# Performance work log

Measured on AMD Instinct MI355X. Metric: run time of the kernel, lower is better.

## Reference

```python
import jax, jax.numpy as jnp
import numpy as np

PATCH, STRIDE, TOPK, EPS = 16, 8, 8, 1e-8

def _leaky(x):
    return jax.nn.leaky_relu(x, 0.01)

def setup_inputs() -> dict:
    key = jax.random.key(0)
    ks = jax.random.split(key, 12)
    s = 0.05  # small weight scale to avoid tanh saturation
    return {
        "X":      jax.random.normal(ks[0], (16, 4096, 512), jnp.float32),
        "W_enc1": jax.random.normal(ks[1], (512, 256), jnp.float32) * s,
        "b_enc1": jax.random.normal(ks[2], (256,), jnp.float32) * s,
        "W_enc2": jax.random.normal(ks[3], (256, 64), jnp.float32) * s,
        "b_enc2": jax.random.normal(ks[4], (64,), jnp.float32) * s,
        "Wq":     jax.random.normal(ks[5], (64, 64), jnp.float32) * s,
        "Wk":     jax.random.normal(ks[6], (64, 64), jnp.float32) * s,
        "Wv":     jax.random.normal(ks[7], (64, 64), jnp.float32) * s,
        "W_agg":  jax.random.normal(ks[8], (64, 64), jnp.float32) * s,
        "b_agg":  jax.random.normal(ks[9], (64,), jnp.float32) * s,
        "W_dec":  jax.random.normal(ks[10], (64, 512), jnp.float32) * s,
        "b_dec":  jax.random.normal(ks[11], (512,), jnp.float32) * s,
    }

def reference(X, W_enc1, b_enc1, W_enc2, b_enc2, Wq, Wk, Wv, W_agg, b_agg, W_dec, b_dec):
    B, L, D = X.shape
    # var_encoder (dropout-free MLP)
    Xe = _leaky(X @ W_enc1 + b_enc1) @ W_enc2 + b_enc2          # (B, L, d)
    d = Xe.shape[-1]
    # unfold into overlapping patches
    h = (L - PATCH) // STRIDE + 1
    pos = jnp.arange(h)[:, None] * STRIDE + jnp.arange(PATCH)[None, :]  # (h, PATCH)
    patches = Xe[:, pos, :]                                      # (B, h, PATCH, d)
    per_patch = patches.mean(axis=2).reshape(B * h, d)           # (N, d)
    q = per_patch @ Wq
    k = per_patch @ Wk
    v = per_patch @ Wv                                           # (N, hqk)
    qn = q / (jnp.linalg.norm(q, axis=-1, keepdims=True) + EPS)
    kn = k / (jnp.linalg.norm(k, axis=-1, keepdims=True) + EPS)
    # antisymmetric outer product, (N, hqk, hqk)
    M = qn[:, :, None] * kn[:, None, :] - kn[:, :, None] * qn[:, None, :]
    A = jax.nn.relu(jnp.tanh(M))
    n = A.shape[-1]
    # topk pruning along last dim via scatter-style mask
    _, idx = jax.lax.top_k(A, TOPK)                              # (N, n, TOPK)
    mask = jnp.any(idx[..., None] == jnp.arange(n), axis=-2)     # (N, n, n) bool
    A = A * mask.astype(A.dtype)
    A = A / jnp.maximum(A.sum(axis=-1, keepdims=True), EPS)
    Av = jnp.einsum('nij,nj->ni', A, v)                          # (N, hqk)
    # after_agg (dropout = identity in eval)
    z = _leaky(Av @ W_agg + b_agg)                               # (N, d)
    zB = z.reshape(B, h, d)
    # overlap-add fold: each patch writes its (constant-over-time) z to its window
    seg = jnp.broadcast_to(zB[:, :, None, :], (B, h, PATCH, d)).reshape(B, h * PATCH, d)
    flat_pos = pos.reshape(-1)                                   # (h*PATCH,)
    out = jnp.zeros((B, L, d), X.dtype).at[:, flat_pos, :].add(seg)
    counts = jnp.zeros((L,), X.dtype).at[flat_pos].add(1.0)
    out = out / jnp.maximum(counts, 1.0)[None, :, None]
    return out @ W_dec + b_dec                                   # (B, L, D)
```

## Files before the change

kernel.cpp:

```cpp
#include <hip/hip_runtime.h>


typedef __attribute__((ext_vector_type(8))) _Float16 half8;
typedef __attribute__((ext_vector_type(4))) _Float16 half4;
typedef __attribute__((ext_vector_type(4))) float floatx4;

__device__ __forceinline__ _Float16 f2h(float f) { return (_Float16)f; }

__global__ __launch_bounds__(256) void prep_weights(
    const float* __restrict__ W1, const float* __restrict__ W2,
    const float* __restrict__ Wd,
    _Float16* __restrict__ W1t, _Float16* __restrict__ W2t,
    _Float16* __restrict__ Wdt)
{
    int idx = blockIdx.x * 256 + threadIdx.x;
    { int n = idx >> 9, k = idx & 511;  W1t[idx] = f2h(W1[k * 256 + n]); }
    if (idx < 16384) { int n = idx >> 8, k = idx & 255; W2t[idx] = f2h(W2[k * 64 + n]); }
    if (idx < 32768) { int n = idx >> 6, k = idx & 63;  Wdt[idx] = f2h(Wd[k * 512 + n]); }
}

template<int BM, int BN, int WM, int WN, bool AF32, int EPI>
__global__ __launch_bounds__(256) void gemm_kernel(
    const void* __restrict__ Aq, const _Float16* __restrict__ Bt,
    const float* __restrict__ bias, void* __restrict__ Cq,
    int M, int N, int K, int lda)
{
    constexpr int LDK = 72;
    __shared__ _Float16 As[BM * LDK];
    __shared__ _Float16 Bs[BN * LDK];
    static_assert(32 * BN * 4 <= BM * LDK * 2, "epilogue chunk must fit in As");

    const int tid  = threadIdx.x;
    const int lane = tid & 63;
    const int w    = tid >> 6;
    constexpr int MWAVES = BM / WM;
    const int wrow = (w % MWAVES) * WM;
    const int wcol = (w / MWAVES) * WN;
    constexpr int MI = WM / 16, NI = WN / 16;
    const int m0 = blockIdx.y * BM;
    const int n0 = blockIdx.x * BN;

    floatx4 acc[MI][NI];
#pragma unroll
    for (int a = 0; a < MI; a++)
#pragma unroll
        for (int bq = 0; bq < NI; bq++) acc[a][bq] = (floatx4){0.f, 0.f, 0.f, 0.f};

    constexpr int EPTA = BM * 64 / 256;
    constexpr int TPRA = 64 / EPTA;
    const int arow  = tid / TPRA;
    const int akseg = (tid % TPRA) * EPTA;
    constexpr int EPTB = BN * 64 / 256;
    constexpr int TPRB = 64 / EPTB;
    const int brow  = tid / TPRB;
    const int bkseg = (tid % TPRB) * EPTB;

    const float*    Af = (const float*)Aq;
    const _Float16* Ah = (const _Float16*)Aq;

    float4 pa[AF32 ? EPTA / 4 : 1];
    half8  paq[AF32 ? 1 : EPTA / 8];
    half8  pb[EPTB / 8];

    auto loadA = [&](int kt) {
        if constexpr (AF32) {
            const float* s = Af + (size_t)(m0 + arow) * lda + kt + akseg;
#pragma unroll
            for (int u = 0; u < EPTA / 4; u++) pa[u] = *(const float4*)(s + 4 * u);
        } else {
            const _Float16* s = Ah + (size_t)(m0 + arow) * lda + kt + akseg;
#pragma unroll
            for (int u = 0; u < EPTA / 8; u++) paq[u] = *(const half8*)(s + 8 * u);
        }
    };
    auto loadB = [&](int kt) {
        const _Float16* s = Bt + (size_t)(n0 + brow) * K + kt + bkseg;
#pragma unroll
        for (int u = 0; u < EPTB / 8; u++) pb[u] = *(const half8*)(s + 8 * u);
    };
    auto stage = [&]() {
        _Float16* d = &As[arow * LDK + akseg];
        if constexpr (AF32) {
#pragma unroll
            for (int u = 0; u < EPTA / 8; u++) {
                float4 f0 = pa[2 * u], f1 = pa[2 * u + 1];
                half8 o;
                o[0] = f2h(f0.x); o[1] = f2h(f0.y); o[2] = f2h(f0.z); o[3] = f2h(f0.w);
                o[4] = f2h(f1.x); o[5] = f2h(f1.y); o[6] = f2h(f1.z); o[7] = f2h(f1.w);
                *(half8*)(d + 8 * u) = o;
            }
        } else {
#pragma unroll
            for (int u = 0; u < EPTA / 8; u++) *(half8*)(d + 8 * u) = paq[u];
        }
        _Float16* db = &Bs[brow * LDK + bkseg];
#pragma unroll
        for (int u = 0; u < EPTB / 8; u++) *(half8*)(db + 8 * u) = pb[u];
    };

    loadA(0); loadB(0);
    for (int kt = 0; kt < K; kt += 64) {
        stage();
        __syncthreads();
        if (kt + 64 < K) { loadA(kt + 64); loadB(kt + 64); }
#pragma unroll
        for (int ks = 0; ks < 2; ks++) {
            const int koff = ks * 32 + (lane >> 4) * 8;
            half8 af[MI], bf[NI];
#pragma unroll
            for (int mi = 0; mi < MI; mi++)
                af[mi] = *(const half8*)&As[(wrow + mi * 16 + (lane & 15)) * LDK + koff];
#pragma unroll
            for (int ni = 0; ni < NI; ni++)
                bf[ni] = *(const half8*)&Bs[(wcol + ni * 16 + (lane & 15)) * LDK + koff];
#pragma unroll
            for (int mi = 0; mi < MI; mi++)
#pragma unroll
                for (int ni = 0; ni < NI; ni++)
                    acc[mi][ni] = __builtin_amdgcn_mfma_f32_16x16x32_f16(
                        af[mi], bf[ni], acc[mi][ni], 0, 0, 0);
        }
        __syncthreads();
    }

    float bvv[NI];
#pragma unroll
    for (int ni = 0; ni < NI; ni++) bvv[ni] = bias[n0 + wcol + ni * 16 + (lane & 15)];

    float* Cs = (float*)As;
#pragma unroll
    for (int c = 0; c < BM / 32; c++) {
        __syncthreads();
        constexpr int DUMMY = 0; (void)DUMMY;
        {
            const int own_wrow = ((c * 32) / WM) * WM;
            if (wrow == own_wrow) {
                constexpr int CPW = 32 < WM ? 32 : WM;
#pragma unroll
                for (int mm = 0; mm < CPW / 16; mm++) {
                    const int mi = ((c * 32) % WM) / 16 + mm;
#pragma unroll
                    for (int ni = 0; ni < NI; ni++) {
#pragma unroll
                        for (int r = 0; r < 4; r++) {
                            const int lr  = mm * 16 + (lane >> 4) * 4 + r;
                            const int col = wcol + ni * 16 + (lane & 15);
                            Cs[lr * BN + col] = acc[mi][ni][r] + bvv[ni];
                        }
                    }
                }
            }
        }
        __syncthreads();
#pragma unroll
        for (int u = 0; u < (32 * BN) / 1024; u++) {
            const int idx = (u * 256 + tid) * 4;
            const int lr = idx / BN, col = idx - lr * BN;
            float4 vv = *(const float4*)&Cs[idx];
            const size_t go = (size_t)(m0 + c * 32 + lr) * N + n0 + col;
            if constexpr (EPI == 0) {
                half4 hv;
                hv[0] = f2h(vv.x > 0.f ? vv.x : 0.01f * vv.x);
                hv[1] = f2h(vv.y > 0.f ? vv.y : 0.01f * vv.y);
                hv[2] = f2h(vv.z > 0.f ? vv.z : 0.01f * vv.z);
                hv[3] = f2h(vv.w > 0.f ? vv.w : 0.01f * vv.w);
                *(half4*)((_Float16*)Cq + go) = hv;
            } else {
                *(float4*)((float*)Cq + go) = vv;
            }
        }
    }
}

#define TOP8_INS(mv) do { float _x = (mv); float _t;            \
    _t = fmaxf(s0,_x); _x = fminf(s0,_x); s0 = _t;              \
    _t = fmaxf(s1,_x); _x = fminf(s1,_x); s1 = _t;              \
    _t = fmaxf(s2,_x); _x = fminf(s2,_x); s2 = _t;              \
    _t = fmaxf(s3,_x); _x = fminf(s3,_x); s3 = _t;              \
    _t = fmaxf(s4,_x); _x = fminf(s4,_x); s4 = _t;              \
    _t = fmaxf(s5,_x); _x = fminf(s5,_x); s5 = _t;              \
    _t = fmaxf(s6,_x); _x = fminf(s6,_x); s6 = _t;              \
    s7 = fmaxf(s7,_x); } while (0)

__global__ __launch_bounds__(256) void patch_attn(
    const float* __restrict__ Xe,  const float* __restrict__ Wq,
    const float* __restrict__ Wk,  const float* __restrict__ Wv,
    const float* __restrict__ Wagg, const float* __restrict__ bagg,
    float* __restrict__ zout)
{
    __shared__ float sh[4][336];
    const int w    = threadIdx.x >> 6;
    const int lane = threadIdx.x & 63;
    const int n = blockIdx.x * 4 + w;
    const int b = n / 511;
    const int i = n - b * 511;
    float* pp  = &sh[w][0];
    float* qs  = pp + 64;
    float* ksm = pp + 128;
    float* vsm = pp + 192;
    float* avs = pp + 256;

    const float* xb = Xe + ((size_t)(b * 4096 + i * 8)) * 64 + lane;
    float s = 0.f;
#pragma unroll
    for (int p = 0; p < 16; p++) s += xb[(size_t)p * 64];
    pp[lane] = s * 0.0625f;
    __syncthreads();

    float q = 0.f, k = 0.f, v = 0.f;
#pragma unroll 4
    for (int e = 0; e < 64; e += 4) {
        float4 p4 = *(const float4*)&pp[e];
        q = fmaf(p4.x, Wq[(e+0)*64+lane], q); q = fmaf(p4.y, Wq[(e+1)*64+lane], q);
        q = fmaf(p4.z, Wq[(e+2)*64+lane], q); q = fmaf(p4.w, Wq[(e+3)*64+lane], q);
        k = fmaf(p4.x, Wk[(e+0)*64+lane], k); k = fmaf(p4.y, Wk[(e+1)*64+lane], k);
        k = fmaf(p4.z, Wk[(e+2)*64+lane], k); k = fmaf(p4.w, Wk[(e+3)*64+lane], k);
        v = fmaf(p4.x, Wv[(e+0)*64+lane], v); v = fmaf(p4.y, Wv[(e+1)*64+lane], v);
        v = fmaf(p4.z, Wv[(e+2)*64+lane], v); v = fmaf(p4.w, Wv[(e+3)*64+lane], v);
    }
    float sq = q * q, sk = k * k;
#pragma unroll
    for (int o = 1; o < 64; o <<= 1) { sq += __shfl_xor(sq, o); sk += __shfl_xor(sk, o); }
    const float qni = q / (sqrtf(sq) + 1e-8f);
    const float kni = k / (sqrtf(sk) + 1e-8f);
    qs[lane] = qni; ksm[lane] = kni; vsm[lane] = v;
    __syncthreads();

    auto MV = [&](float kj, float qj) { return fmaf(qni, kj, -(kni * qj)); };

    float s0=-1e30f,s1=-1e30f,s2=-1e30f,s3=-1e30f,s4=-1e30f,s5=-1e30f,s6=-1e30f,s7=-1e30f;
#pragma unroll
    for (int j = 0; j < 64; j += 4) {
        float4 k4 = *(const float4*)&ksm[j];
        float4 q4 = *(const float4*)&qs[j];
        TOP8_INS(MV(k4.x, q4.x)); TOP8_INS(MV(k4.y, q4.y));
        TOP8_INS(MV(k4.z, q4.z)); TOP8_INS(MV(k4.w, q4.w));
    }
    const float teff = fmaxf(s7, 1e-37f) * (1.f - 1.2e-7f);

    float ssum = 0.f, av = 0.f;
#pragma unroll
    for (int j = 0; j < 64; j += 4) {
        float4 k4 = *(const float4*)&ksm[j];
        float4 q4 = *(const float4*)&qs[j];
        float4 v4 = *(const float4*)&vsm[j];
#define P2(KJ, QJ, VJ) do { float _m = MV(KJ, QJ); float _x2 = _m * _m;           \
        float _a = _m * (15.f + _x2) * __builtin_amdgcn_rcpf(fmaf(6.f, _x2, 15.f)); \
        float _am = (_m >= teff) ? _a : 0.f;                                       \
        ssum += _am; av = fmaf(_am, (VJ), av); } while (0)
        P2(k4.x, q4.x, v4.x); P2(k4.y, q4.y, v4.y);
        P2(k4.z, q4.z, v4.z); P2(k4.w, q4.w, v4.w);
#undef P2
    }
    avs[lane] = av / fmaxf(ssum, 1e-8f);
    __syncthreads();

    float zc = bagg[lane];
#pragma unroll 4
    for (int e = 0; e < 64; e += 4) {
        float4 a4 = *(const float4*)&avs[e];
        zc = fmaf(a4.x, Wagg[(e+0)*64+lane], zc); zc = fmaf(a4.y, Wagg[(e+1)*64+lane], zc);
        zc = fmaf(a4.z, Wagg[(e+2)*64+lane], zc); zc = fmaf(a4.w, Wagg[(e+3)*64+lane], zc);
    }
    zc = zc > 0.f ? zc : 0.01f * zc;
    zout[(size_t)n * 64 + lane] = zc;
}

__global__ __launch_bounds__(256) void scatter_avg(
    const float* __restrict__ z, _Float16* __restrict__ zavg)
{
    const int idx = blockIdx.x * 256 + threadIdx.x;
    const int c = idx & 63;
    const int l = (idx >> 6) & 4095;
    const int b = idx >> 18;
    const int g = l >> 3;
    float s = 0.f, cnt = 0.f;
    if (g >= 1)   { s += z[((size_t)(b * 511 + g - 1)) * 64 + c]; cnt += 1.f; }
    if (g <= 510) { s += z[((size_t)(b * 511 + g)) * 64 + c];     cnt += 1.f; }
    zavg[idx] = f2h(s / cnt);
}

extern "C" void kernel_launch(void* const* d_in, const int* in_sizes, int n_in,
                              void* d_out, int out_size, void* d_ws, size_t ws_size,
                              hipStream_t stream)
{
    const float* X    = (const float*)d_in[0];
    const float* W1   = (const float*)d_in[1];
    const float* b1   = (const float*)d_in[2];
    const float* W2   = (const float*)d_in[3];
    const float* b2   = (const float*)d_in[4];
    const float* Wq   = (const float*)d_in[5];
    const float* Wk   = (const float*)d_in[6];
    const float* Wv   = (const float*)d_in[7];
    const float* Wagg = (const float*)d_in[8];
    const float* bagg = (const float*)d_in[9];
    const float* Wd   = (const float*)d_in[10];
    const float* bd   = (const float*)d_in[11];

    char* ws = (char*)d_ws;
    _Float16* hidden = (_Float16*)(ws);
    float*    Xe     = (float*)(ws + 33554432);
    float*    z      = (float*)(ws + 50331648);
    _Float16* zavg   = (_Float16*)(ws + 52424704);
    _Float16* W1t    = (_Float16*)(ws + 60813312);
    _Float16* W2t    = (_Float16*)(ws + 61075456);
    _Float16* Wdt    = (_Float16*)(ws + 61108224);
    float* out = (float*)d_out;

    prep_weights<<<512, 256, 0, stream>>>(W1, W2, Wd, W1t, W2t, Wdt);

    gemm_kernel<128,128,64,64,true,0><<<dim3(2,512), 256, 0, stream>>>(
        X, W1t, b1, hidden, 65536, 256, 512, 512);
    gemm_kernel<128,64,32,64,false,1><<<dim3(1,512), 256, 0, stream>>>(
        hidden, W2t, b2, Xe, 65536, 64, 256, 256);
    patch_attn<<<2044, 256, 0, stream>>>(Xe, Wq, Wk, Wv, Wagg, bagg, z);
    scatter_avg<<<16384, 256, 0, stream>>>(z, zavg);
    gemm_kernel<128,128,64,64,false,1><<<dim3(4,512), 256, 0, stream>>>(
        zavg, Wdt, bd, out, 65536, 512, 64, 64);
}
```

Baseline: 341.2 us.

## Fuse encoder GEMMs in one kernel and fold scatter-average into decoder

Merges the two encoder GEMMs into one kernel. Each block computes a 64-row hidden tile (all 256 columns) and keeps it in shared memory for the second GEMM, so the fp16 hidden tensor never goes through global memory. W1 tiles are loaded straight into LDS with global_load_lds using an XOR swizzle. The overlap-add averaging is computed inside the decoder's A-tile load, which removes the scatter_avg kernel and the zavg buffer. The costs are higher shared-memory use per block and a less parallel grid for the first GEMM, since each block now covers all 256 columns.

```diff
diff --git a/kernel.cpp b/kernel.cpp
--- a/kernel.cpp
+++ b/kernel.cpp
@@ -6,6 +6,8 @@
 typedef __attribute__((ext_vector_type(4))) float floatx4;
 
 __device__ __forceinline__ _Float16 f2h(float f) { return (_Float16)f; }
+
+#define MFMA16(A, B, C) __builtin_amdgcn_mfma_f32_16x16x32_f16((A), (B), (C), 0, 0, 0)
 
 __global__ __launch_bounds__(256) void prep_weights(
     const float* __restrict__ W1, const float* __restrict__ W2,
@@ -19,155 +21,136 @@
     if (idx < 32768) { int n = idx >> 6, k = idx & 63;  Wdt[idx] = f2h(Wd[k * 512 + n]); }
 }
 
-template<int BM, int BN, int WM, int WN, bool AF32, int EPI>
-__global__ __launch_bounds__(256) void gemm_kernel(
-    const void* __restrict__ Aq, const _Float16* __restrict__ Bt,
-    const float* __restrict__ bias, void* __restrict__ Cq,
-    int M, int N, int K, int lda)
-{
-    constexpr int LDK = 72;
-    __shared__ _Float16 As[BM * LDK];
-    __shared__ _Float16 Bs[BN * LDK];
-    static_assert(32 * BN * 4 <= BM * LDK * 2, "epilogue chunk must fit in As");
+__global__ __launch_bounds__(256) void enc_fused(
+    const float* __restrict__ X, const _Float16* __restrict__ W1t,
+    const float* __restrict__ b1, const _Float16* __restrict__ W2t,
+    const float* __restrict__ b2, float* __restrict__ Xe)
+{
+    __shared__ _Float16 smem[21504];
+    _Float16* As  = smem;
+    _Float16* Bs  = smem + 4608;
+    _Float16* Hs  = smem;
+    _Float16* W2s = smem + 16896;
 
     const int tid  = threadIdx.x;
     const int lane = tid & 63;
     const int w    = tid >> 6;
-    constexpr int MWAVES = BM / WM;
-    const int wrow = (w % MWAVES) * WM;
-    const int wcol = (w / MWAVES) * WN;
-    constexpr int MI = WM / 16, NI = WN / 16;
-    const int m0 = blockIdx.y * BM;
-    const int n0 = blockIdx.x * BN;
-
-    floatx4 acc[MI][NI];
-#pragma unroll
-    for (int a = 0; a < MI; a++)
-#pragma unroll
-        for (int bq = 0; bq < NI; bq++) acc[a][bq] = (floatx4){0.f, 0.f, 0.f, 0.f};
-
-    constexpr int EPTA = BM * 64 / 256;
-    constexpr int TPRA = 64 / EPTA;
-    const int arow  = tid / TPRA;
-    const int akseg = (tid % TPRA) * EPTA;
-    constexpr int EPTB = BN * 64 / 256;
-    constexpr int TPRB = 64 / EPTB;
-    const int brow  = tid / TPRB;
-    const int bkseg = (tid % TPRB) * EPTB;
-
-    const float*    Af = (const float*)Aq;
-    const _Float16* Ah = (const _Float16*)Aq;
-
-    float4 pa[AF32 ? EPTA / 4 : 1];
-    half8  paq[AF32 ? 1 : EPTA / 8];
-    half8  pb[EPTB / 8];
-
+    const int m0   = blockIdx.x * 64;
+
+    const int arow  = tid >> 2;
+    const int akseg = (tid & 3) << 4;
+    const float* Abase = X + (size_t)(m0 + arow) * 512 + akseg;
+
+    const int brow0  = (w << 6) + (lane >> 3);
+    const int bchunk = (((lane & 7) ^ ((lane >> 3) & 7)) << 3);
+
+    floatx4 acc1[4][4];
+#pragma unroll
+    for (int ci = 0; ci < 4; ci++)
+#pragma unroll
+        for (int mi = 0; mi < 4; mi++) acc1[ci][mi] = (floatx4){0.f, 0.f, 0.f, 0.f};
+
+    float4 pa[4];
     auto loadA = [&](int kt) {
-        if constexpr (AF32) {
-            const float* s = Af + (size_t)(m0 + arow) * lda + kt + akseg;
-#pragma unroll
-            for (int u = 0; u < EPTA / 4; u++) pa[u] = *(const float4*)(s + 4 * u);
-        } else {
-            const _Float16* s = Ah + (size_t)(m0 + arow) * lda + kt + akseg;
-#pragma unroll
-            for (int u = 0; u < EPTA / 8; u++) paq[u] = *(const half8*)(s + 8 * u);
-        }
+#pragma unroll
+        for (int u = 0; u < 4; u++) pa[u] = *(const float4*)(Abase + kt + 4 * u);
     };
-    auto loadB = [&](int kt) {
-        const _Float16* s = Bt + (size_t)(n0 + brow) * K + kt + bkseg;
-#pragma unroll
-        for (int u = 0; u < EPTB / 8; u++) pb[u] = *(const half8*)(s + 8 * u);
-    };
-    auto stage = [&]() {
-        _Float16* d = &As[arow * LDK + akseg];
-        if constexpr (AF32) {
-#pragma unroll
-            for (int u = 0; u < EPTA / 8; u++) {
-                float4 f0 = pa[2 * u], f1 = pa[2 * u + 1];
+
+    loadA(0);
+    for (int kt = 0; kt < 512; kt += 64) {
+#pragma unroll
+        for (int inst = 0; inst < 8; inst++) {
+            const _Float16* src = W1t + (size_t)(brow0 + inst * 8) * 512 + kt + bchunk;
+            __builtin_amdgcn_global_load_lds(
+                (const __attribute__((address_space(1))) unsigned int*)src,
+                (__attribute__((address_space(3))) unsigned int*)(Bs + ((w << 6) + inst * 8) * 64),
+                16, 0, 0);
+        }
+        {
+            _Float16* d = &As[arow * 72 + akseg];
+#pragma unroll
+            for (int h = 0; h < 2; h++) {
+                float4 f0 = pa[2 * h], f1 = pa[2 * h + 1];
                 half8 o;
                 o[0] = f2h(f0.x); o[1] = f2h(f0.y); o[2] = f2h(f0.z); o[3] = f2h(f0.w);
                 o[4] = f2h(f1.x); o[5] = f2h(f1.y); o[6] = f2h(f1.z); o[7] = f2h(f1.w);
-                *(half8*)(d + 8 * u) = o;
+                *(half8*)(d + 8 * h) = o;
             }
-        } else {
-#pragma unroll
-            for (int u = 0; u < EPTA / 8; u++) *(half8*)(d + 8 * u) = paq[u];
-        }
-        _Float16* db = &Bs[brow * LDK + bkseg];
-#pragma unroll
-        for (int u = 0; u < EPTB / 8; u++) *(half8*)(db + 8 * u) = pb[u];
-    };
-
-    loadA(0); loadB(0);
-    for (int kt = 0; kt < K; kt += 64) {
-        stage();
-        __syncthreads();
-        if (kt + 64 < K) { loadA(kt + 64); loadB(kt + 64); }
+        }
+        __syncthreads();
+        if (kt + 64 < 512) loadA(kt + 64);
 #pragma unroll
         for (int ks = 0; ks < 2; ks++) {
-            const int koff = ks * 32 + (lane >> 4) * 8;
-            half8 af[MI], bf[NI];
-#pragma unroll
-            for (int mi = 0; mi < MI; mi++)
-                af[mi] = *(const half8*)&As[(wrow + mi * 16 + (lane & 15)) * LDK + koff];
-#pragma unroll
-            for (int ni = 0; ni < NI; ni++)
-                bf[ni] = *(const half8*)&Bs[(wcol + ni * 16 + (lane & 15)) * LDK + koff];
-#pragma unroll
-            for (int mi = 0; mi < MI; mi++)
-#pragma unroll
-                for (int ni = 0; ni < NI; ni++)
-                    acc[mi][ni] = __builtin_amdgcn_mfma_f32_16x16x32_f16(
-                        af[mi], bf[ni], acc[mi][ni], 0, 0, 0);
-        }
-        __syncthreads();
-    }
-
-    float bvv[NI];
-#pragma unroll
-    for (int ni = 0; ni < NI; ni++) bvv[ni] = bias[n0 + wcol + ni * 16 + (lane & 15)];
-
-    float* Cs = (float*)As;
-#pragma unroll
-    for (int c = 0; c < BM / 32; c++) {
-        __syncthreads();
-        constexpr int DUMMY = 0; (void)DUMMY;
-        {
-            const int own_wrow = ((c * 32) / WM) * WM;
-            if (wrow == own_wrow) {
-                constexpr int CPW = 32 < WM ? 32 : WM;
-#pragma unroll
-                for (int mm = 0; mm < CPW / 16; mm++) {
-                    const int mi = ((c * 32) % WM) / 16 + mm;
-#pragma unroll
-                    for (int ni = 0; ni < NI; ni++) {
-#pragma unroll
-                        for (int r = 0; r < 4; r++) {
-                            const int lr  = mm * 16 + (lane >> 4) * 4 + r;
-                            const int col = wcol + ni * 16 + (lane & 15);
-                            Cs[lr * BN + col] = acc[mi][ni][r] + bvv[ni];
-                        }
-                    }
-                }
+            const int lchunk = ks * 4 + (lane >> 4);
+            half8 af[4], bf[4];
+#pragma unroll
+            for (int ci = 0; ci < 4; ci++) {
+                const int c = (w << 6) + ci * 16 + (lane & 15);
+                af[ci] = *(const half8*)&Bs[c * 64 + ((lchunk ^ (lane & 7)) << 3)];
             }
-        }
-        __syncthreads();
-#pragma unroll
-        for (int u = 0; u < (32 * BN) / 1024; u++) {
-            const int idx = (u * 256 + tid) * 4;
-            const int lr = idx / BN, col = idx - lr * BN;
-            float4 vv = *(const float4*)&Cs[idx];
-            const size_t go = (size_t)(m0 + c * 32 + lr) * N + n0 + col;
-            if constexpr (EPI == 0) {
-                half4 hv;
-                hv[0] = f2h(vv.x > 0.f ? vv.x : 0.01f * vv.x);
-                hv[1] = f2h(vv.y > 0.f ? vv.y : 0.01f * vv.y);
-                hv[2] = f2h(vv.z > 0.f ? vv.z : 0.01f * vv.z);
-                hv[3] = f2h(vv.w > 0.f ? vv.w : 0.01f * vv.w);
-                *(half4*)((_Float16*)Cq + go) = hv;
-            } else {
-                *(float4*)((float*)Cq + go) = vv;
+#pragma unroll
+            for (int mi = 0; mi < 4; mi++)
+                bf[mi] = *(const half8*)&As[(mi * 16 + (lane & 15)) * 72 + ks * 32 + ((lane >> 4) << 3)];
+#pragma unroll
+            for (int ci = 0; ci < 4; ci++)
+#pragma unroll
+                for (int mi = 0; mi < 4; mi++)
+                    acc1[ci][mi] = MFMA16(af[ci], bf[mi], acc1[ci][mi]);
+        }
+        __syncthreads();
+    }
+
+    float4 b1v[4];
+#pragma unroll
+    for (int ci = 0; ci < 4; ci++)
+        b1v[ci] = *(const float4*)&b1[(w << 6) + ci * 16 + ((lane >> 4) << 2)];
+#pragma unroll
+    for (int ci = 0; ci < 4; ci++) {
+        const int cb = (w << 6) + ci * 16 + ((lane >> 4) << 2);
+#pragma unroll
+        for (int mi = 0; mi < 4; mi++) {
+            const int m = mi * 16 + (lane & 15);
+            half4 hv;
+#pragma unroll
+            for (int r = 0; r < 4; r++) {
+                float v = acc1[ci][mi][r] + ((const float*)&b1v[ci])[r];
+                v = v > 0.f ? v : 0.01f * v;
+                hv[r] = f2h(v);
             }
+            *(half4*)&Hs[m * 264 + cb] = hv;
+        }
+    }
+
+    floatx4 acc2[4];
+#pragma unroll
+    for (int ni = 0; ni < 4; ni++) acc2[ni] = (floatx4){0.f, 0.f, 0.f, 0.f};
+    const int w2n   = tid >> 2;
+    const int w2seg = (tid & 3) << 4;
+#pragma unroll
+    for (int p = 0; p < 4; p++) {
+        *(half8*)&W2s[w2n * 72 + w2seg]     = *(const half8*)&W2t[w2n * 256 + p * 64 + w2seg];
+        *(half8*)&W2s[w2n * 72 + w2seg + 8] = *(const half8*)&W2t[w2n * 256 + p * 64 + w2seg + 8];
+        __syncthreads();
+#pragma unroll
+        for (int ks = 0; ks < 2; ks++) {
+            half8 a2 = *(const half8*)&Hs[((w << 4) + (lane & 15)) * 264 + p * 64 + ks * 32 + ((lane >> 4) << 3)];
+            half8 b2f[4];
+#pragma unroll
+            for (int ni = 0; ni < 4; ni++)
+                b2f[ni] = *(const half8*)&W2s[(ni * 16 + (lane & 15)) * 72 + ks * 32 + ((lane >> 4) << 3)];
+#pragma unroll
+            for (int ni = 0; ni < 4; ni++)
+                acc2[ni] = MFMA16(a2, b2f[ni], acc2[ni]);
+        }
+        __syncthreads();
+    }
+#pragma unroll
+    for (int ni = 0; ni < 4; ni++) {
+        const float bb = b2[ni * 16 + (lane & 15)];
+#pragma unroll
+        for (int r = 0; r < 4; r++) {
+            const int row = m0 + (w << 4) + ((lane >> 4) << 2) + r;
+            Xe[(size_t)row * 64 + ni * 16 + (lane & 15)] = acc2[ni][r] + bb;
         }
     }
 }
@@ -266,18 +249,116 @@
     zout[(size_t)n * 64 + lane] = zc;
 }
 
-__global__ __launch_bounds__(256) void scatter_avg(
-    const float* __restrict__ z, _Float16* __restrict__ zavg)
-{
-    const int idx = blockIdx.x * 256 + threadIdx.x;
-    const int c = idx & 63;
-    const int l = (idx >> 6) & 4095;
-    const int b = idx >> 18;
-    const int g = l >> 3;
-    float s = 0.f, cnt = 0.f;
-    if (g >= 1)   { s += z[((size_t)(b * 511 + g - 1)) * 64 + c]; cnt += 1.f; }
-    if (g <= 510) { s += z[((size_t)(b * 511 + g)) * 64 + c];     cnt += 1.f; }
-    zavg[idx] = f2h(s / cnt);
+__global__ __launch_bounds__(256) void dec_fused(
+    const float* __restrict__ z, const _Float16* __restrict__ Wdt,
+    const float* __restrict__ bd, float* __restrict__ out)
+{
+    __shared__ _Float16 As[128 * 72];
+    __shared__ _Float16 Bs[128 * 72];
+    const int tid  = threadIdx.x;
+    const int lane = tid & 63;
+    const int w    = tid >> 6;
+    const int m0 = blockIdx.y * 128, n0 = blockIdx.x * 128;
+    const int wrow = (w & 1) << 6, wcol = (w >> 1) << 6;
+
+    {
+        const int arow  = tid >> 1;
+        const int akseg = (tid & 1) << 5;
+        const int row = m0 + arow;
+        const int b = row >> 12, l = row & 4095, g = l >> 3;
+        const int g0 = g - 1 >= 0 ? g - 1 : 0;
+        const int g1 = g <= 510 ? g : 510;
+        const float w0 = (g >= 1) ? 1.f : 0.f;
+        const float w1 = (g <= 510) ? 1.f : 0.f;
+        const float sc = (w0 + w1) > 1.5f ? 0.5f : 1.f;
+        const float* z0 = z + ((size_t)(b * 511 + g0)) * 64 + akseg;
+        const float* z1 = z + ((size_t)(b * 511 + g1)) * 64 + akseg;
+        _Float16* d = &As[arow * 72 + akseg];
+#pragma unroll
+        for (int u = 0; u < 4; u++) {
+            float4 f0a = *(const float4*)(z0 + 8 * u);
+            float4 f0b = *(const float4*)(z0 + 8 * u + 4);
+            float4 f1a = *(const float4*)(z1 + 8 * u);
+            float4 f1b = *(const float4*)(z1 + 8 * u + 4);
+            half8 o;
+            o[0] = f2h((f0a.x * w0 + f1a.x * w1) * sc);
+            o[1] = f2h((f0a.y * w0 + f1a.y * w1) * sc);
+            o[2] = f2h((f0a.z * w0 + f1a.z * w1) * sc);
+            o[3] = f2h((f0a.w * w0 + f1a.w * w1) * sc);
+            o[4] = f2h((f0b.x * w0 + f1b.x * w1) * sc);
+            o[5] = f2h((f0b.y * w0 + f1b.y * w1) * sc);
+            o[6] = f2h((f0b.z * w0 + f1b.z * w1) * sc);
+            o[7] = f2h((f0b.w * w0 + f1b.w * w1) * sc);
+            *(half8*)(d + 8 * u) = o;
+        }
+    }
+    {
+        const int brow  = tid >> 1;
+        const int bkseg = (tid & 1) << 5;
+        const _Float16* s = Wdt + (size_t)(n0 + brow) * 64 + bkseg;
+        _Float16* d = &Bs[brow * 72 + bkseg];
+#pragma unroll
+        for (int u = 0; u < 4; u++) *(half8*)(d + 8 * u) = *(const half8*)(s + 8 * u);
+    }
+    __syncthreads();
+
+    floatx4 acc[2][4];
+    floatx4 accf[4][4];
+#pragma unroll
+    for (int mi = 0; mi < 4; mi++)
+#pragma unroll
+        for (int ni = 0; ni < 4; ni++) accf[mi][ni] = (floatx4){0.f, 0.f, 0.f, 0.f};
+    (void)acc;
+#pragma unroll
+    for (int ks = 0; ks < 2; ks++) {
+        const int koff = ks * 32 + ((lane >> 4) << 3);
+        half8 af[4], bf[4];
+#pragma unroll
+        for (int mi = 0; mi < 4; mi++)
+            af[mi] = *(const half8*)&As[(wrow + mi * 16 + (lane & 15)) * 72 + koff];
+#pragma unroll
+        for (int ni = 0; ni < 4; ni++)
+            bf[ni] = *(const half8*)&Bs[(wcol + ni * 16 + (lane & 15)) * 72 + koff];
+#pragma unroll
+        for (int mi = 0; mi < 4; mi++)
+#pragma unroll
+            for (int ni = 0; ni < 4; ni++)
+                accf[mi][ni] = MFMA16(af[mi], bf[ni], accf[mi][ni]);
+    }
+
+    float bvv[4];
+#pragma unroll
+    for (int ni = 0; ni < 4; ni++) bvv[ni] = bd[n0 + wcol + ni * 16 + (lane & 15)];
+
+    float* Cs = (float*)As;
+#pragma unroll
+    for (int c = 0; c < 4; c++) {
+        __syncthreads();
+        const int own_wrow = ((c * 32) / 64) * 64;
+        if (wrow == own_wrow) {
+#pragma unroll
+            for (int mm = 0; mm < 2; mm++) {
+                const int mi = ((c * 32) % 64) / 16 + mm;
+#pragma unroll
+                for (int ni = 0; ni < 4; ni++) {
+#pragma unroll
+                    for (int r = 0; r < 4; r++) {
+                        const int lr  = mm * 16 + ((lane >> 4) << 2) + r;
+                        const int col = wcol + ni * 16 + (lane & 15);
+                        Cs[lr * 128 + col] = accf[mi][ni][r] + bvv[ni];
+                    }
+                }
+            }
+        }
+        __syncthreads();
+#pragma unroll
+        for (int u = 0; u < 4; u++) {
+            const int idx = (u * 256 + tid) * 4;
+            const int lr = idx >> 7, col = idx & 127;
+            float4 vv = *(const float4*)&Cs[idx];
+            *(float4*)&out[(size_t)(m0 + c * 32 + lr) * 512 + n0 + col] = vv;
+        }
+    }
 }
 
 extern "C" void kernel_launch(void* const* d_in, const int* in_sizes, int n_in,
@@ -298,23 +379,15 @@
     const float* bd   = (const float*)d_in[11];
 
     char* ws = (char*)d_ws;
-    _Float16* hidden = (_Float16*)(ws);
-    float*    Xe     = (float*)(ws + 33554432);
-    float*    z      = (float*)(ws + 50331648);
-    _Float16* zavg   = (_Float16*)(ws + 52424704);
-    _Float16* W1t    = (_Float16*)(ws + 60813312);
-    _Float16* W2t    = (_Float16*)(ws + 61075456);
-    _Float16* Wdt    = (_Float16*)(ws + 61108224);
+    float*    Xe  = (float*)(ws);
+    float*    z   = (float*)(ws + 16777216);
+    _Float16* W1t = (_Float16*)(ws + 18870272);
+    _Float16* W2t = (_Float16*)(ws + 19132416);
+    _Float16* Wdt = (_Float16*)(ws + 19165184);
     float* out = (float*)d_out;
 
     prep_weights<<<512, 256, 0, stream>>>(W1, W2, Wd, W1t, W2t, Wdt);
-
-    gemm_kernel<128,128,64,64,true,0><<<dim3(2,512), 256, 0, stream>>>(
-        X, W1t, b1, hidden, 65536, 256, 512, 512);
-    gemm_kernel<128,64,32,64,false,1><<<dim3(1,512), 256, 0, stream>>>(
-        hidden, W2t, b2, Xe, 65536, 64, 256, 256);
+    enc_fused<<<1024, 256, 0, stream>>>(X, W1t, b1, W2t, b2, Xe);
     patch_attn<<<2044, 256, 0, stream>>>(Xe, Wq, Wk, Wv, Wagg, bagg, z);
-    scatter_avg<<<16384, 256, 0, stream>>>(z, zavg);
-    gemm_kernel<128,128,64,64,false,1><<<dim3(4,512), 256, 0, stream>>>(
-        zavg, Wdt, bd, out, 65536, 512, 64, 64);
-}
+    dec_fused<<<dim3(4, 512), 256, 0, stream>>>(z, Wdt, bd, out);
+}
```

After: 318.3 us. 6.7% less time.
